# Kernel tuning notes

Hardware: AMD Instinct MI355X
Metric: run time of the kernel (lower is better)

Reference implementation:

```python
import jax, jax.numpy as jnp
import numpy as np

IN_F, OUT_F, K = 512, 512, 3
UP = 1
EPS = 1e-08
LR_MUL = 1.0
PAD = (K - 1) // 2
C_EQ = LR_MUL / np.sqrt(IN_F * K * K)  # EqualizedWeight scale


def setup_inputs() -> dict:
    key = jax.random.key(0)
    k1, k2, k3, k4 = jax.random.split(key, 4)
    b, h, w = 16, 64, 64
    x = jax.random.normal(k1, (b, IN_F, h, w), dtype=jnp.float32)
    s = jax.random.uniform(k2, (b, IN_F), dtype=jnp.float32)
    weight = jax.random.normal(k3, (OUT_F, IN_F, K, K), dtype=jnp.float32)
    bias = jax.random.normal(k4, (OUT_F,), dtype=jnp.float32)
    return {"x": x, "s": s, "weight": weight, "bias": bias}


def _conv_one(xi, wi):
    # xi: [c,h,w], wi: [out,in,k,k]
    out = jax.lax.conv_general_dilated(
        xi[None], wi,
        window_strides=(1, 1),
        padding=[(PAD, PAD), (PAD, PAD)],
        dimension_numbers=("NCHW", "OIHW", "NCHW"),
    )
    return out[0]


def reference(x, s, weight, bias):
    # modulate: [b,out,in,k,k]
    w = (weight * C_EQ)[None] * s[:, None, :, None, None]
    # demodulate
    sigma_inv = jax.lax.rsqrt(jnp.sum(w * w, axis=(2, 3, 4), keepdims=True) + EPS)
    w = w * sigma_inv
    # per-sample conv (equivalent to grouped conv with groups=b)
    out = jax.vmap(_conv_one)(x, w)  # [b,out,h,w]
    out = out + (bias * LR_MUL)[None, :, None, None]
    return out
```

## Files before the change

kernel.cpp:

```cpp
#include <hip/hip_runtime.h>
#include <cstdint>

typedef unsigned short u16;
typedef __bf16 bf16x8 __attribute__((ext_vector_type(8)));
typedef float f32x4 __attribute__((ext_vector_type(4)));

#define B_    16
#define CIN   512
#define COUT  512
#define HW_   64
#define PW    66
#define XH_ELEMS ((size_t)B_*PW*PW*CIN)
#define WA_ELEMS ((size_t)B_*16*9*COUT*32)

__device__ __forceinline__ float bf2f(u16 v) {
  union { unsigned int u; float f; } c; c.u = ((unsigned int)v) << 16; return c.f;
}
__device__ __forceinline__ u16 f2bf(float f) {
  union { float f; unsigned int u; } c; c.f = f;
  unsigned int u = c.u + 0x7fffu + ((c.u >> 16) & 1u);
  return (u16)(u >> 16);
}

__device__ __forceinline__ void async16(const void* g, void* l) {
  __builtin_amdgcn_global_load_lds(
      (__attribute__((address_space(1))) unsigned int*)(uintptr_t)g,
      (__attribute__((address_space(3))) unsigned int*)(uintptr_t)l,
      16, 0, 0);
}

__global__ __launch_bounds__(256) void zero_border(u16* __restrict__ xh) {
  int g = blockIdx.x * 256 + threadIdx.x;
  if (g >= B_ * 260 * 64) return;
  int c8 = g & 63;
  int t  = g >> 6;
  int b  = t / 260;
  int p  = t - b * 260;
  int rp, cp;
  if (p < 66)       { rp = 0;      cp = p; }
  else if (p < 132) { rp = 65;     cp = p - 66; }
  else {
    int q = p - 132;
    if (q < 64) { rp = q + 1;  cp = 0; }
    else        { rp = q - 63; cp = 65; }
  }
  u16* dst = xh + ((((size_t)b * PW + rp) * PW + cp) << 9) + (c8 << 3);
  *(uint4*)dst = make_uint4(0u, 0u, 0u, 0u);
}

__global__ __launch_bounds__(256) void transpose_x(const float* __restrict__ x,
                                                   u16* __restrict__ xh) {
  __shared__ u16 tile[64][72];
  const int b  = blockIdx.z;
  const int y  = blockIdx.y;
  const int i0 = blockIdx.x * 64;
  const int t  = threadIdx.x;

  const int ciL = t >> 4;
  const int xg  = (t & 15) * 4;
#pragma unroll
  for (int u = 0; u < 4; ++u) {
    const int ci = ciL + u * 16;
    const float4 v = *(const float4*)(
        x + ((((size_t)b * CIN + i0 + ci) * HW_ + y) * HW_ + xg));
    u16* d = &tile[ci][xg];
    d[0] = f2bf(v.x); d[1] = f2bf(v.y); d[2] = f2bf(v.z); d[3] = f2bf(v.w);
  }
  __syncthreads();

  const int xx = t >> 2;
  const int cg = (t & 3) * 16;
  u16 outv[16];
#pragma unroll
  for (int u = 0; u < 16; ++u) outv[u] = tile[cg + u][xx];
  u16* dst = xh + ((((size_t)b * PW + (y + 1)) * PW + (xx + 1)) << 9) + i0 + cg;
  *(uint4*)dst       = *(uint4*)&outv[0];
  *(uint4*)(dst + 8) = *(uint4*)&outv[8];
}

__global__ __launch_bounds__(256) void mod_weights(const float* __restrict__ w,
                                                   const float* __restrict__ s,
                                                   u16* __restrict__ wA) {
  const int gwid = (blockIdx.x * 256 + threadIdx.x) >> 6;
  const int lane = threadIdx.x & 63;
  const int b = gwid >> 9;
  const int o = gwid & 511;
  const float* wrow = w + (size_t)o * (CIN * 9);
  const float* srow = s + (size_t)b * CIN;

  float acc = 0.f;
  float sv[8];
#pragma unroll
  for (int j = 0; j < 8; ++j) {
    const int i = lane + j * 64;
    const float si = srow[i];
    sv[j] = si;
    const float* wp = wrow + i * 9;
    float q = 0.f;
#pragma unroll
    for (int t = 0; t < 9; ++t) { float wv = wp[t]; q += wv * wv; }
    acc += si * si * q;
  }
#pragma unroll
  for (int off = 32; off > 0; off >>= 1) acc += __shfl_xor(acc, off, 64);

  const float C_EQ = 1.4731391e-2f;
  const float sigma_inv = rsqrtf(acc * (C_EQ * C_EQ) + 1e-8f);

  u16* base = wA + (size_t)b * (16 * 9 * COUT * 32);
#pragma unroll
  for (int j = 0; j < 8; ++j) {
    const int i = lane + j * 64;
    const float scale = C_EQ * sv[j] * sigma_inv;
    const float* wp = wrow + i * 9;
    const int icc = i >> 5, ich = i & 31;
#pragma unroll
    for (int t = 0; t < 9; ++t) {
      base[(((icc * 9 + t) * COUT) + o) * 32 + ich] = f2bf(wp[t] * scale);
    }
  }
}

#define AS_ELEMS (128 * 32)
#define BROWS    (6 * 66)
#define BS_ELEMS (BROWS * 32)

__device__ __forceinline__ void stage_A(const u16* __restrict__ wb,
                                        u16* dst, int phase, int o0, int tid) {
  const u16* asrc = wb + ((size_t)phase * COUT + o0) * 32;
#pragma unroll
  for (int t = 0; t < 2; ++t) {
    const int id   = t * 256 + tid;
    const int row  = id >> 2;
    const int slot = (id & 3) ^ (row & 3);
    async16(asrc + row * 32 + slot * 8, dst + id * 8);
  }
}

__device__ __forceinline__ void stage_B_slice(const u16* __restrict__ xb,
                                              u16* dst, int ic, int y0,
                                              int tid, int slice) {
  if (tid < 198) {
    const int id   = slice * 198 + tid;
    const int row  = id >> 2;
    const int slot = (id & 3) ^ (row & 3);
    async16(xb + ((size_t)y0 * PW + row) * CIN + ic * 32 + slot * 8,
            dst + id * 8);
  }
}

__global__ __launch_bounds__(256, 2) void modconv_mfma(const u16* __restrict__ xh,
                                                       const u16* __restrict__ wA,
                                                       const float* __restrict__ bias,
                                                       float* __restrict__ out) {
  __shared__ u16 As[2 * AS_ELEMS];
  __shared__ u16 Bs[2 * BS_ELEMS];

  const int tid  = threadIdx.x;
  const int lane = tid & 63;
  const int wv   = tid >> 6;
  const int l15  = lane & 15;
  const int q    = lane >> 4;
  const int sw15 = l15 & 3;

  const int lin     = blockIdx.x;
  const int logical = ((lin & 7) << 7) + (lin >> 3);
  const int yt = logical & 15;
  const int ot = (logical >> 4) & 3;
  const int b  = logical >> 6;
  const int y0 = yt << 2;
  const int o0 = ot << 7;

  const u16* xb = xh + (size_t)b * (PW * PW * CIN);
  const u16* wb = wA + (size_t)b * (16 * 9 * COUT * 32);

  f32x4 acc[8][4];
#pragma unroll
  for (int mi = 0; mi < 8; ++mi)
#pragma unroll
    for (int cg = 0; cg < 4; ++cg) acc[mi][cg] = (f32x4){0.f, 0.f, 0.f, 0.f};

#pragma unroll
  for (int s = 0; s < 8; ++s) stage_B_slice(xb, Bs, 0, y0, tid, s);
  stage_A(wb, As, 0, o0, tid);

  for (int ic = 0; ic < 16; ++ic) {
    const int icp   = ic & 1;
    const int bOff  = icp * BS_ELEMS;
    const int bOffN = BS_ELEMS - bOff;
#pragma unroll
    for (int tap = 0; tap < 9; ++tap) {
      __syncthreads();

      const int aCur = (((ic + tap) & 1) ? AS_ELEMS : 0);
      const int aNxt = AS_ELEMS - aCur;
      if (!(ic == 15 && tap == 8))
        stage_A(wb, As + aNxt, ic * 9 + tap + 1, o0, tid);
      if (ic < 15 && tap < 8)
        stage_B_slice(xb, Bs + bOffN, ic + 1, y0, tid, tap);

      const int ky = tap / 3, kx = tap % 3;
      const int rbbase = (wv + ky) * 66 + kx;

      bf16x8 bfr[4];
#pragma unroll
      for (int cg = 0; cg < 4; ++cg) {
        const int rb = rbbase + cg * 16 + l15;
        bfr[cg] = *(const bf16x8*)
          &Bs[bOff + (rb << 5) + ((q ^ (rb & 3)) << 3)];
      }

      __builtin_amdgcn_s_setprio(1);
#pragma unroll
      for (int mi = 0; mi < 8; ++mi) {
        const int ra = (mi << 4) + l15;
        const bf16x8 af = *(const bf16x8*)
          &As[aCur + (ra << 5) + ((q ^ sw15) << 3)];
#pragma unroll
        for (int cg = 0; cg < 4; ++cg)
          acc[mi][cg] = __builtin_amdgcn_mfma_f32_16x16x32_bf16(
              af, bfr[cg], acc[mi][cg], 0, 0, 0);
      }
      __builtin_amdgcn_s_setprio(0);
    }
  }

  const int y = y0 + wv;
#pragma unroll
  for (int mi = 0; mi < 8; ++mi) {
#pragma unroll
    for (int rg = 0; rg < 4; ++rg) {
      const int o = o0 + (mi << 4) + (q << 2) + rg;
      const float bv = bias[o];
      const size_t base = (((size_t)b * COUT + o) * HW_ + y) * HW_;
#pragma unroll
      for (int cg = 0; cg < 4; ++cg)
        out[base + (cg << 4) + l15] = acc[mi][cg][rg] + bv;
    }
  }
}

extern "C" void kernel_launch(void* const* d_in, const int* in_sizes, int n_in,
                              void* d_out, int out_size, void* d_ws, size_t ws_size,
                              hipStream_t stream) {
  const float* x    = (const float*)d_in[0];
  const float* s    = (const float*)d_in[1];
  const float* w    = (const float*)d_in[2];
  const float* bias = (const float*)d_in[3];
  float* out = (float*)d_out;

  u16* xh = (u16*)d_ws;
  u16* wA = xh + XH_ELEMS;

  zero_border<<<(B_ * 260 * 64 + 255) / 256, 256, 0, stream>>>(xh);
  transpose_x<<<dim3(8, 64, 16), 256, 0, stream>>>(x, xh);
  mod_weights<<<2048, 256, 0, stream>>>(w, s, wA);
  modconv_mfma<<<1024, 256, 0, stream>>>(xh, wA, bias, out);
}
```

Before: 529.5 us.

## Triple-buffer weight tiles with vmcnt waits and split weight modulation kernel

The conv main loop now keeps three weight stages in LDS and issues prefetches two taps ahead. It replaces the full __syncthreads with explicit vmcnt waits plus a raw barrier, and peels the last input-channel block into its own loop. The weight-modulation kernel is split in two: one computes per-(batch,out) demodulation factors, reading each weight row once and reusing it across all batches. The other stages weight tiles in LDS and writes coalesced 16-byte bf16 stores instead of scattered 2-byte ones. The sigma buffer borrows the output tensor as scratch, and the hand-tuned vmcnt counts risk races if they don't match the number of loads in flight.

```diff
diff --git a/kernel.cpp b/kernel.cpp
--- a/kernel.cpp
+++ b/kernel.cpp
@@ -13,9 +13,8 @@
 #define XH_ELEMS ((size_t)B_*PW*PW*CIN)
 #define WA_ELEMS ((size_t)B_*16*9*COUT*32)
 
-__device__ __forceinline__ float bf2f(u16 v) {
-  union { unsigned int u; float f; } c; c.u = ((unsigned int)v) << 16; return c.f;
-}
+#define WAITV(N) asm volatile("s_waitcnt vmcnt(" #N ")" ::: "memory")
+
 __device__ __forceinline__ u16 f2bf(float f) {
   union { float f; unsigned int u; } c; c.f = f;
   unsigned int u = c.u + 0x7fffu + ((c.u >> 16) & 1u);
@@ -78,46 +77,82 @@
   *(uint4*)(dst + 8) = *(uint4*)&outv[8];
 }
 
-__global__ __launch_bounds__(256) void mod_weights(const float* __restrict__ w,
-                                                   const float* __restrict__ s,
-                                                   u16* __restrict__ wA) {
-  const int gwid = (blockIdx.x * 256 + threadIdx.x) >> 6;
+__global__ __launch_bounds__(256) void sigma_kernel(const float* __restrict__ w,
+                                                    const float* __restrict__ s,
+                                                    float* __restrict__ sig) {
+  const int o    = blockIdx.x * 4 + (threadIdx.x >> 6);
   const int lane = threadIdx.x & 63;
-  const int b = gwid >> 9;
-  const int o = gwid & 511;
   const float* wrow = w + (size_t)o * (CIN * 9);
-  const float* srow = s + (size_t)b * CIN;
-
-  float acc = 0.f;
-  float sv[8];
+
+  float q[8];
 #pragma unroll
   for (int j = 0; j < 8; ++j) {
-    const int i = lane + j * 64;
-    const float si = srow[i];
-    sv[j] = si;
-    const float* wp = wrow + i * 9;
-    float q = 0.f;
-#pragma unroll
-    for (int t = 0; t < 9; ++t) { float wv = wp[t]; q += wv * wv; }
-    acc += si * si * q;
-  }
-#pragma unroll
-  for (int off = 32; off > 0; off >>= 1) acc += __shfl_xor(acc, off, 64);
-
+    const float* wp = wrow + (lane + j * 64) * 9;
+    float qq = 0.f;
+#pragma unroll
+    for (int t = 0; t < 9; ++t) { const float wv = wp[t]; qq += wv * wv; }
+    q[j] = qq;
+  }
   const float C_EQ = 1.4731391e-2f;
-  const float sigma_inv = rsqrtf(acc * (C_EQ * C_EQ) + 1e-8f);
+#pragma unroll
+  for (int b = 0; b < 16; ++b) {
+    const float* srow = s + (size_t)b * CIN;
+    float acc = 0.f;
+#pragma unroll
+    for (int j = 0; j < 8; ++j) {
+      const float si = srow[lane + j * 64];
+      acc += si * si * q[j];
+    }
+#pragma unroll
+    for (int off = 32; off > 0; off >>= 1) acc += __shfl_xor(acc, off, 64);
+    if (lane == 0) sig[b * COUT + o] = rsqrtf(acc * (C_EQ * C_EQ) + 1e-8f);
+  }
+}
+
+__global__ __launch_bounds__(256, 2) void scale_weights(const float* __restrict__ w,
+                                                        const float* __restrict__ s,
+                                                        const float* __restrict__ sig,
+                                                        u16* __restrict__ wA) {
+  __shared__ float wld[64 * 292];
+  __shared__ float s2[32];
+  __shared__ float si[64];
+
+  const int tid = threadIdx.x;
+  const int lin = blockIdx.x;
+  const int l   = ((lin & 7) << 8) + (lin >> 3);
+  const int b   = l & 15;
+  const int sid = l >> 4;
+  const int icc = sid & 15;
+  const int oq  = sid >> 4;
+  const int o0  = oq << 6;
+
+#pragma unroll
+  for (int k = 0; k < 18; ++k) {
+    const int c   = k * 256 + tid;
+    const int ol  = c / 72;
+    const int col = c - ol * 72;
+    const float4 v = *(const float4*)(
+        w + ((size_t)(o0 + ol) * 512 + icc * 32) * 9 + col * 4);
+    *(float4*)&wld[ol * 292 + col * 4] = v;
+  }
+  if (tid < 32) s2[tid] = 1.4731391e-2f * s[(size_t)b * CIN + icc * 32 + tid];
+  else if (tid < 96) si[tid - 32] = sig[(size_t)b * COUT + o0 + (tid - 32)];
+  __syncthreads();
 
   u16* base = wA + (size_t)b * (16 * 9 * COUT * 32);
 #pragma unroll
-  for (int j = 0; j < 8; ++j) {
-    const int i = lane + j * 64;
-    const float scale = C_EQ * sv[j] * sigma_inv;
-    const float* wp = wrow + i * 9;
-    const int icc = i >> 5, ich = i & 31;
-#pragma unroll
-    for (int t = 0; t < 9; ++t) {
-      base[(((icc * 9 + t) * COUT) + o) * 32 + ich] = f2bf(wp[t] * scale);
-    }
+  for (int tap = 0; tap < 9; ++tap) {
+    const int ol = tid >> 2;
+    const int g  = tid & 3;
+    const float sg = si[ol];
+    u16 outc[8];
+#pragma unroll
+    for (int kk = 0; kk < 8; ++kk) {
+      const int i = g * 8 + kk;
+      outc[kk] = f2bf(wld[ol * 292 + i * 9 + tap] * s2[i] * sg);
+    }
+    *(uint4*)(base + (((size_t)(icc * 9 + tap) * COUT) + o0 + ol) * 32 + g * 8)
+        = *(uint4*)outc;
   }
 }
 
@@ -153,7 +188,7 @@
                                                        const u16* __restrict__ wA,
                                                        const float* __restrict__ bias,
                                                        float* __restrict__ out) {
-  __shared__ u16 As[2 * AS_ELEMS];
+  __shared__ u16 As[3 * AS_ELEMS];
   __shared__ u16 Bs[2 * BS_ELEMS];
 
   const int tid  = threadIdx.x;
@@ -181,25 +216,22 @@
     for (int cg = 0; cg < 4; ++cg) acc[mi][cg] = (f32x4){0.f, 0.f, 0.f, 0.f};
 
 #pragma unroll
-  for (int s = 0; s < 8; ++s) stage_B_slice(xb, Bs, 0, y0, tid, s);
+  for (int sl = 0; sl < 8; ++sl) stage_B_slice(xb, Bs, 0, y0, tid, sl);
   stage_A(wb, As, 0, o0, tid);
-
-  for (int ic = 0; ic < 16; ++ic) {
-    const int icp   = ic & 1;
-    const int bOff  = icp * BS_ELEMS;
-    const int bOffN = BS_ELEMS - bOff;
+  stage_A(wb, As + AS_ELEMS, 1, o0, tid);
+
+  for (int ic = 0; ic < 15; ++ic) {
+    const int bOff = (ic & 1) * BS_ELEMS;
+    const int bNxt = BS_ELEMS - bOff;
 #pragma unroll
     for (int tap = 0; tap < 9; ++tap) {
-      __syncthreads();
-
-      const int aCur = (((ic + tap) & 1) ? AS_ELEMS : 0);
-      const int aNxt = AS_ELEMS - aCur;
-      if (!(ic == 15 && tap == 8))
-        stage_A(wb, As + aNxt, ic * 9 + tap + 1, o0, tid);
-      if (ic < 15 && tap < 8)
-        stage_B_slice(xb, Bs + bOffN, ic + 1, y0, tid, tap);
+      if (tap == 0) { WAITV(2); } else { WAITV(3); }
+      __builtin_amdgcn_s_barrier();
+      __builtin_amdgcn_sched_barrier(0);
 
       const int ky = tap / 3, kx = tap % 3;
+      const int aCur = (tap % 3) * AS_ELEMS;
+      const int aDst = ((tap + 2) % 3) * AS_ELEMS;
       const int rbbase = (wv + ky) * 66 + kx;
 
       bf16x8 bfr[4];
@@ -209,6 +241,47 @@
         bfr[cg] = *(const bf16x8*)
           &Bs[bOff + (rb << 5) + ((q ^ (rb & 3)) << 3)];
       }
+
+      stage_A(wb, As + aDst, ic * 9 + tap + 2, o0, tid);
+      if (tap < 8) stage_B_slice(xb, Bs + bNxt, ic + 1, y0, tid, tap);
+
+      __builtin_amdgcn_s_setprio(1);
+#pragma unroll
+      for (int mi = 0; mi < 8; ++mi) {
+        const int ra = (mi << 4) + l15;
+        const bf16x8 af = *(const bf16x8*)
+          &As[aCur + (ra << 5) + ((q ^ sw15) << 3)];
+#pragma unroll
+        for (int cg = 0; cg < 4; ++cg)
+          acc[mi][cg] = __builtin_amdgcn_mfma_f32_16x16x32_bf16(
+              af, bfr[cg], acc[mi][cg], 0, 0, 0);
+      }
+      __builtin_amdgcn_s_setprio(0);
+    }
+  }
+
+  {
+    const int bOff = BS_ELEMS;
+#pragma unroll
+    for (int tap = 0; tap < 9; ++tap) {
+      if (tap < 8) { WAITV(2); } else { WAITV(0); }
+      __builtin_amdgcn_s_barrier();
+      __builtin_amdgcn_sched_barrier(0);
+
+      const int ky = tap / 3, kx = tap % 3;
+      const int aCur = (tap % 3) * AS_ELEMS;
+      const int rbbase = (wv + ky) * 66 + kx;
+
+      bf16x8 bfr[4];
+#pragma unroll
+      for (int cg = 0; cg < 4; ++cg) {
+        const int rb = rbbase + cg * 16 + l15;
+        bfr[cg] = *(const bf16x8*)
+          &Bs[bOff + (rb << 5) + ((q ^ (rb & 3)) << 3)];
+      }
+
+      if (tap <= 6)
+        stage_A(wb, As + ((tap + 2) % 3) * AS_ELEMS, 135 + tap + 2, o0, tid);
 
       __builtin_amdgcn_s_setprio(1);
 #pragma unroll
@@ -251,9 +324,11 @@
 
   u16* xh = (u16*)d_ws;
   u16* wA = xh + XH_ELEMS;
+  float* sig = (float*)d_out;
 
   zero_border<<<(B_ * 260 * 64 + 255) / 256, 256, 0, stream>>>(xh);
   transpose_x<<<dim3(8, 64, 16), 256, 0, stream>>>(x, xh);
-  mod_weights<<<2048, 256, 0, stream>>>(w, s, wA);
+  sigma_kernel<<<128, 256, 0, stream>>>(w, s, sig);
+  scale_weights<<<2048, 256, 0, stream>>>(w, s, sig, wA);
   modconv_mfma<<<1024, 256, 0, stream>>>(xh, wA, bias, out);
 }
```

Measured after the change: 484.4 us. 8.5% less time.
